# Performance work log

Hardware: AMD Instinct MI355X
Metric: run time of the kernel (lower is better)

## Reference

```python
import jax, jax.numpy as jnp
import numpy as np


def setup_inputs() -> dict:
    key = jax.random.key(0)
    kq, kk, kv = jax.random.split(key, 3)
    B, H, N, D = 2, 16, 2048, 128
    q = jax.random.normal(kq, (B, H, N, D), dtype=jnp.float32)
    k = jax.random.normal(kk, (B, H, N, D), dtype=jnp.float32)
    v = jax.random.normal(kv, (B, H, N, D), dtype=jnp.float32)
    return {"q": q, "k": k, "v": v, "num_sink": 4, "window_size": 1024}


def reference(q, k, v, num_sink, window_size):
    # Sink + sliding-window causal attention (single-device path of the SP wrapper).
    # Query i attends to key j iff j <= i AND (j < num_sink OR i - j < window_size).
    B, H, N, D = q.shape
    scale = 1.0 / np.sqrt(D).astype(np.float32)
    i = jnp.arange(N)[:, None]   # query positions
    j = jnp.arange(N)[None, :]   # key positions
    mask = (j <= i) & ((j < num_sink) | ((i - j) < window_size))  # [N, N]
    scores = jnp.einsum('bhid,bhjd->bhij', q, k) * scale          # [B,H,N,N]
    scores = jnp.where(mask, scores, jnp.finfo(scores.dtype).min)
    attn = jax.nn.softmax(scores, axis=-1)
    return jnp.einsum('bhij,bhjd->bhid', attn, v)
```

## Files before the change

### kernel.cpp

```cpp
#include <hip/hip_runtime.h>
#include <stdint.h>

#define NN 2048
#define DD 128
#define BHH 32
#define QT 64
#define KT 64

typedef short v8s __attribute__((ext_vector_type(8)));
typedef short v4s __attribute__((ext_vector_type(4)));
typedef float v4f __attribute__((ext_vector_type(4)));
typedef unsigned int u32;
typedef u32 u32x2 __attribute__((ext_vector_type(2)));
typedef u32 u32x4 __attribute__((ext_vector_type(4)));

__device__ __forceinline__ unsigned short f2bf(float x) {
  unsigned u = __builtin_bit_cast(unsigned, x);
  u += 0x7fffu + ((u >> 16) & 1u);
  return (unsigned short)(u >> 16);
}

__device__ __forceinline__ v8s cvt8(const float* __restrict__ p) {
  v8s r;
#pragma unroll
  for (int j = 0; j < 8; j++) r[j] = (short)f2bf(p[j]);
  return r;
}

__device__ __forceinline__ u32 pk2(float a, float b) {
  u32 r;
  asm("v_cvt_pk_bf16_f32 %0, %1, %2" : "=v"(r) : "v"(a), "v"(b));
  return r;
}

__global__ __launch_bounds__(256) void prep(const float* __restrict__ K, const float* __restrict__ V,
                     unsigned short* __restrict__ Kb, unsigned short* __restrict__ Vt) {
  const int z = blockIdx.z;
  const int tid = threadIdx.x;
  if (z >= BHH) {
    const int bh = z - BHH;
    const int chunk = blockIdx.y * 32 + blockIdx.x;
    size_t base = (size_t)bh * NN * DD + (size_t)chunk * 4096 + (size_t)tid * 16;
    v4f f0 = *(const v4f*)(K + base);
    v4f f1 = *(const v4f*)(K + base + 4);
    v4f f2 = *(const v4f*)(K + base + 8);
    v4f f3 = *(const v4f*)(K + base + 12);
    u32x4 w0 = { pk2(f0[0], f0[1]), pk2(f0[2], f0[3]), pk2(f1[0], f1[1]), pk2(f1[2], f1[3]) };
    u32x4 w1 = { pk2(f2[0], f2[1]), pk2(f2[2], f2[3]), pk2(f3[0], f3[1]), pk2(f3[2], f3[3]) };
    *(u32x4*)(Kb + base) = w0;
    *(u32x4*)(Kb + base + 8) = w1;
    return;
  }
  __shared__ __align__(16) unsigned short t[64 * 68];
  const int bh = z;
  const int n0 = blockIdx.x * 64, d0 = blockIdx.y * 64;
  const int c16 = tid & 15, r4 = tid >> 4;
  const float* src = V + ((size_t)bh * NN + n0 + r4 * 4) * DD + d0 + c16 * 4;
  v4f f0 = *(const v4f*)(src);
  v4f f1 = *(const v4f*)(src + DD);
  v4f f2 = *(const v4f*)(src + 2 * DD);
  v4f f3 = *(const v4f*)(src + 3 * DD);
#pragma unroll
  for (int j = 0; j < 4; j++) {
    u32x2 w = { pk2(f0[j], f1[j]), pk2(f2[j], f3[j]) };
    *(u32x2*)(t + (c16 * 4 + j) * 68 + r4 * 4) = w;
  }
  __syncthreads();
  unsigned short* dst = Vt + ((size_t)bh * DD + d0) * NN + n0;
#pragma unroll
  for (int p = 0; p < 2; p++) {
    int d = p * 32 + (tid >> 3);
    int nc = (tid & 7) * 8;
    v4s x0 = *(const v4s*)(t + d * 68 + nc);
    v4s x1 = *(const v4s*)(t + d * 68 + nc + 4);
    v8s o = { x0[0], x0[1], x0[2], x0[3], x1[0], x1[1], x1[2], x1[3] };
    *(v8s*)(dst + (size_t)d * NN + nc) = o;
  }
}

template <bool PREPPED>
__global__ __launch_bounds__(256, 3) void attn(
    const float* __restrict__ Q,
    const float* __restrict__ Kf, const unsigned short* __restrict__ Kb,
    const unsigned short* __restrict__ Vt, const float* __restrict__ Vf,
    const int* __restrict__ nsp, const int* __restrict__ wsp,
    float* __restrict__ O) {
  const int ns = nsp[0], win = wsp[0];
  const int x = blockIdx.x;
  const int xcd = x & 7, slot = x >> 3;
  const int bh = xcd + 8 * (slot / 24);
  const int jobid = slot % 24;
  int qis[2], njobs;
  if (jobid < 16) { njobs = 1; qis[0] = 31 - jobid; qis[1] = 0; }
  else { int p = jobid - 16; njobs = 2; qis[0] = 15 - p; qis[1] = p; }

  const int tid = threadIdx.x;
  const int w = tid >> 6;
  const int l = tid & 63;
  const int lo = l & 15, q4 = l >> 4;

  __shared__ __align__(16) unsigned short Kl[64 * 128];
  __shared__ __align__(16) unsigned short Vl[64 * 128];
  __shared__ __align__(16) unsigned short Pl[4 * 1024];
  unsigned short* Pw = Pl + w * 1024;
  const int prd = q4 * 128 + lo * 8;

  const float csc = 0.088388347648318447f * 1.4426950408889634f;

  const size_t koff0 = ((size_t)bh * NN + w * 16 + lo) * DD + q4 * 8;
  const unsigned short* vtb = Vt + (size_t)bh * DD * NN;

  for (int ji = 0; ji < njobs; ji++) {
    const int q0 = qis[ji] * QT;
    const int qrow0 = q0 + w * 16;
    const int qi = qrow0 + lo;

    v8s qf[4];
    {
      const float* qb = Q + ((size_t)bh * NN + qrow0 + lo) * DD + q4 * 8;
#pragma unroll
      for (int kc = 0; kc < 4; kc++) {
        v8s r;
#pragma unroll
        for (int e = 0; e < 8; e++) r[e] = (short)f2bf(qb[kc * 32 + e] * csc);
        qf[kc] = r;
      }
    }

    float lsum = 0.f;
    v4f oa[8];
#pragma unroll
    for (int nc = 0; nc < 8; nc++) oa[nc] = (v4f){0.f, 0.f, 0.f, 0.f};

    const int wstart = q0 - win + 1;
    const bool sink16 = (wstart > KT - 1) && (ns <= 16);
    const int kb_lo = sink16 ? ((wstart >> 6) << 6) : 0;
    const int kb_hi = q0 + QT;

    v8s kst[4], vst[4];
    auto stage_load = [&](int kb) {
      const size_t g = koff0 + (size_t)kb * DD;
#pragma unroll
      for (int kc = 0; kc < 4; kc++)
        kst[kc] = PREPPED ? *(const v8s*)(Kb + g + kc * 32) : cvt8(Kf + g + kc * 32);
#pragma unroll
      for (int i = 0; i < 4; i++) {
        const int f = w * 4 + i, kt = f >> 3, nc = f & 7;
        if constexpr (PREPPED) {
          vst[i] = *(const v8s*)(vtb + ((size_t)nc * 16 + lo) * NN + kb + kt * 32 + q4 * 8);
        } else {
          v8s r;
#pragma unroll
          for (int e = 0; e < 8; e++)
            r[e] = (short)f2bf(Vf[((size_t)bh * NN + kb + kt * 32 + q4 * 8 + e) * DD + nc * 16 + lo]);
          vst[i] = r;
        }
      }
    };

    stage_load(kb_lo);

    if (sink16) {
      v8s kf0[4];
      const size_t g0 = ((size_t)bh * NN + lo) * DD + q4 * 8;
#pragma unroll
      for (int kc = 0; kc < 4; kc++)
        kf0[kc] = PREPPED ? *(const v8s*)(Kb + g0 + kc * 32) : cvt8(Kf + g0 + kc * 32);
      v4f s0 = (v4f){0.f, 0.f, 0.f, 0.f};
#pragma unroll
      for (int kc = 0; kc < 4; kc++)
        s0 = __builtin_amdgcn_mfma_f32_16x16x32_bf16(kf0[kc], qf[kc], s0, 0, 0, 0);
#pragma unroll
      for (int r = 0; r < 4; r++) {
        const int kj = q4 * 4 + r;
        const bool valid = (kj < ns) && (kj <= qi);
        s0[r] = valid ? __builtin_amdgcn_exp2f(s0[r]) : 0.f;
      }
      lsum += (s0[0] + s0[1]) + (s0[2] + s0[3]);
      u32x2 pw = { pk2(s0[0], s0[1]), pk2(s0[2], s0[3]) };
      *(u32x2*)(Pw + (q4 >> 1) * 128 + lo * 8 + (q4 & 1) * 4) = pw;
      u32x2 pz = { 0u, 0u };
      *(u32x2*)(Pw + (2 + (q4 >> 1)) * 128 + lo * 8 + (q4 & 1) * 4) = pz;
      v8s pf = *(const v8s*)(Pw + prd);
#pragma unroll
      for (int nc = 0; nc < 8; nc++) {
        v8s vf;
        if constexpr (PREPPED)
          vf = *(const v8s*)(vtb + ((size_t)nc * 16 + lo) * NN + q4 * 8);
        else {
          v8s r;
#pragma unroll
          for (int e = 0; e < 8; e++)
            r[e] = (short)f2bf(Vf[((size_t)bh * NN + q4 * 8 + e) * DD + nc * 16 + lo]);
          vf = r;
        }
        oa[nc] = __builtin_amdgcn_mfma_f32_16x16x32_bf16(pf, vf, oa[nc], 0, 0, 0);
      }
    }

    for (int kb = kb_lo; kb < kb_hi; kb += KT) {
      __syncthreads();
#pragma unroll
      for (int kc = 0; kc < 4; kc++)
        *(v8s*)(Kl + (w * 4 + kc) * 512 + l * 8) = kst[kc];
#pragma unroll
      for (int i = 0; i < 4; i++)
        *(v8s*)(Vl + (w * 4 + i) * 512 + l * 8) = vst[i];
      __syncthreads();
      if (kb + KT < kb_hi) stage_load(kb + KT);

      v4f s[4];
      __builtin_amdgcn_s_setprio(1);
#pragma unroll
      for (int ct = 0; ct < 4; ct++) {
        s[ct] = (v4f){0.f, 0.f, 0.f, 0.f};
#pragma unroll
        for (int kc = 0; kc < 4; kc++) {
          v8s kf = *(const v8s*)(Kl + (ct * 4 + kc) * 512 + l * 8);
          s[ct] = __builtin_amdgcn_mfma_f32_16x16x32_bf16(kf, qf[kc], s[ct], 0, 0, 0);
        }
      }
      __builtin_amdgcn_s_setprio(0);

      const bool full = (kb + KT - 1 <= qrow0) && (kb + win >= qrow0 + 16);
      if (full) {
#pragma unroll
        for (int ct = 0; ct < 4; ct++)
#pragma unroll
          for (int r = 0; r < 4; r++) s[ct][r] = __builtin_amdgcn_exp2f(s[ct][r]);
      } else {
#pragma unroll
        for (int ct = 0; ct < 4; ct++) {
          const int kjb = kb + ct * 16 + q4 * 4;
#pragma unroll
          for (int r = 0; r < 4; r++) {
            const int kj = kjb + r;
            const bool valid = (kj <= qi) && ((kj < ns) || (qi - kj < win));
            s[ct][r] = valid ? __builtin_amdgcn_exp2f(s[ct][r]) : 0.f;
          }
        }
      }
#pragma unroll
      for (int ct = 0; ct < 4; ct++)
        lsum += (s[ct][0] + s[ct][1]) + (s[ct][2] + s[ct][3]);

#pragma unroll
      for (int ct = 0; ct < 4; ct++) {
        u32x2 pw = { pk2(s[ct][0], s[ct][1]), pk2(s[ct][2], s[ct][3]) };
        *(u32x2*)(Pw + (ct >> 1) * 512 + ((ct & 1) * 2 + (q4 >> 1)) * 128 + lo * 8 + (q4 & 1) * 4) = pw;
      }
#pragma unroll
      for (int kt = 0; kt < 2; kt++) {
        v8s pf = *(const v8s*)(Pw + kt * 512 + prd);
        __builtin_amdgcn_s_setprio(1);
#pragma unroll
        for (int nc = 0; nc < 8; nc++) {
          v8s vf = *(const v8s*)(Vl + (kt * 8 + nc) * 512 + l * 8);
          oa[nc] = __builtin_amdgcn_mfma_f32_16x16x32_bf16(pf, vf, oa[nc], 0, 0, 0);
        }
        __builtin_amdgcn_s_setprio(0);
      }
    }

    float lt = lsum;
    lt += __shfl_xor(lt, 16, 64);
    lt += __shfl_xor(lt, 32, 64);
    const float inv = 1.f / lt;
    float invr[4];
#pragma unroll
    for (int r = 0; r < 4; r++) invr[r] = __shfl(inv, (l & 48) | (q4 * 4 + r), 64);
    float* ob = O + ((size_t)bh * NN + qrow0) * DD;
#pragma unroll
    for (int nc = 0; nc < 8; nc++)
#pragma unroll
      for (int r = 0; r < 4; r++)
        ob[(size_t)(q4 * 4 + r) * DD + nc * 16 + lo] = oa[nc][r] * invr[r];
  }
}

extern "C" void kernel_launch(void* const* d_in, const int* in_sizes, int n_in,
                              void* d_out, int out_size, void* d_ws, size_t ws_size,
                              hipStream_t stream) {
  const float* q = (const float*)d_in[0];
  const float* k = (const float*)d_in[1];
  const float* v = (const float*)d_in[2];
  const int* nsp = (const int*)d_in[3];
  const int* wsp = (const int*)d_in[4];
  float* out = (float*)d_out;

  const size_t half = (size_t)BHH * NN * DD * sizeof(unsigned short);
  const int nblocks = BHH * 24;

  if (ws_size >= 2 * half) {
    unsigned short* kbf = (unsigned short*)d_ws;
    unsigned short* vt = (unsigned short*)((char*)d_ws + half);
    prep<<<dim3(32, 2, 2 * BHH), 256, 0, stream>>>(k, v, kbf, vt);
    attn<true><<<nblocks, 256, 0, stream>>>(q, k, kbf, vt, v, nsp, wsp, out);
  } else {
    attn<false><<<nblocks, 256, 0, stream>>>(q, k, nullptr, nullptr, v, nsp, wsp, out);
  }
}
```

Measured before the change: 194.0 us.

## Switch attention to 32x32x16 MFMA with two 32-row waves and register P transpose

Rewrites the attention kernel to use 32x32x16 bf16 MFMA instead of 16x16x32, with 128-thread blocks where each of two waves owns 32 query rows. The P matrix is repacked into the A-operand layout in registers via permlane32_swap instead of round-tripping through shared memory, removing the P LDS buffer. This cuts per-MFMA instruction overhead and LDS traffic but doubles per-wave register state (qf, kst/vst, accumulators) and halves threads per block, which may reduce occupancy and latency hiding.

```diff
diff --git a/kernel.cpp b/kernel.cpp
--- a/kernel.cpp
+++ b/kernel.cpp
@@ -10,6 +10,7 @@
 typedef short v8s __attribute__((ext_vector_type(8)));
 typedef short v4s __attribute__((ext_vector_type(4)));
 typedef float v4f __attribute__((ext_vector_type(4)));
+typedef float v16f __attribute__((ext_vector_type(16)));
 typedef unsigned int u32;
 typedef u32 u32x2 __attribute__((ext_vector_type(2)));
 typedef u32 u32x4 __attribute__((ext_vector_type(4)));
@@ -79,7 +80,7 @@
 }
 
 template <bool PREPPED>
-__global__ __launch_bounds__(256, 3) void attn(
+__global__ __launch_bounds__(128, 2) void attn(
     const float* __restrict__ Q,
     const float* __restrict__ Kf, const unsigned short* __restrict__ Kb,
     const unsigned short* __restrict__ Vt, const float* __restrict__ Vf,
@@ -97,62 +98,73 @@
   const int tid = threadIdx.x;
   const int w = tid >> 6;
   const int l = tid & 63;
-  const int lo = l & 15, q4 = l >> 4;
-
-  __shared__ __align__(16) unsigned short Kl[64 * 128];
-  __shared__ __align__(16) unsigned short Vl[64 * 128];
-  __shared__ __align__(16) unsigned short Pl[4 * 1024];
-  unsigned short* Pw = Pl + w * 1024;
-  const int prd = q4 * 128 + lo * 8;
+  const int m = l & 31;
+  const int hi = l >> 5;
+  const int rbase = 4 * hi;
+
+  __shared__ __align__(16) unsigned short Kl[16 * 512];
+  __shared__ __align__(16) unsigned short Vl[16 * 512];
 
   const float csc = 0.088388347648318447f * 1.4426950408889634f;
 
-  const size_t koff0 = ((size_t)bh * NN + w * 16 + lo) * DD + q4 * 8;
+  const size_t kK = ((size_t)bh * NN + w * 32 + m) * DD + hi * 8;
   const unsigned short* vtb = Vt + (size_t)bh * DD * NN;
+
+  auto mkpa = [&](float a0, float a1, float a2, float a3,
+                  float b0, float b1, float b2, float b3) -> v8s {
+    u32x2 r02 = __builtin_amdgcn_permlane32_swap(pk2(a0, a1), pk2(b0, b1), false, false);
+    u32x2 r13 = __builtin_amdgcn_permlane32_swap(pk2(a2, a3), pk2(b2, b3), false, false);
+    u32x4 pw = { r02[0], r13[0], r02[1], r13[1] };
+    return __builtin_bit_cast(v8s, pw);
+  };
 
   for (int ji = 0; ji < njobs; ji++) {
     const int q0 = qis[ji] * QT;
-    const int qrow0 = q0 + w * 16;
-    const int qi = qrow0 + lo;
-
-    v8s qf[4];
+    const int qrow0w = q0 + w * 32;
+    const int qi = qrow0w + m;
+
+    v8s qf[8];
     {
-      const float* qb = Q + ((size_t)bh * NN + qrow0 + lo) * DD + q4 * 8;
-#pragma unroll
-      for (int kc = 0; kc < 4; kc++) {
+      const float* qb = Q + ((size_t)bh * NN + qi) * DD + hi * 8;
+#pragma unroll
+      for (int kc = 0; kc < 8; kc++) {
         v8s r;
 #pragma unroll
-        for (int e = 0; e < 8; e++) r[e] = (short)f2bf(qb[kc * 32 + e] * csc);
+        for (int e = 0; e < 8; e++) r[e] = (short)f2bf(qb[kc * 16 + e] * csc);
         qf[kc] = r;
       }
     }
 
     float lsum = 0.f;
-    v4f oa[8];
-#pragma unroll
-    for (int nc = 0; nc < 8; nc++) oa[nc] = (v4f){0.f, 0.f, 0.f, 0.f};
+    v16f oa[4];
+#pragma unroll
+    for (int nc = 0; nc < 4; nc++) oa[nc] = (v16f)(0.f);
 
     const int wstart = q0 - win + 1;
     const bool sink16 = (wstart > KT - 1) && (ns <= 16);
     const int kb_lo = sink16 ? ((wstart >> 6) << 6) : 0;
     const int kb_hi = q0 + QT;
 
-    v8s kst[4], vst[4];
+    v8s kst[8], vst[8];
     auto stage_load = [&](int kb) {
-      const size_t g = koff0 + (size_t)kb * DD;
-#pragma unroll
-      for (int kc = 0; kc < 4; kc++)
-        kst[kc] = PREPPED ? *(const v8s*)(Kb + g + kc * 32) : cvt8(Kf + g + kc * 32);
-#pragma unroll
-      for (int i = 0; i < 4; i++) {
-        const int f = w * 4 + i, kt = f >> 3, nc = f & 7;
+#pragma unroll
+      for (int i = 0; i < 8; i++) {
         if constexpr (PREPPED) {
-          vst[i] = *(const v8s*)(vtb + ((size_t)nc * 16 + lo) * NN + kb + kt * 32 + q4 * 8);
+          kst[i] = *(const v8s*)(Kb + kK + (size_t)kb * DD + i * 16);
+        } else {
+          kst[i] = cvt8(Kf + kK + (size_t)kb * DD + i * 16);
+        }
+      }
+#pragma unroll
+      for (int i = 0; i < 8; i++) {
+        const int kt = w * 2 + (i >> 2), nc = i & 3;
+        if constexpr (PREPPED) {
+          vst[i] = *(const v8s*)(vtb + ((size_t)nc * 32 + m) * NN + kb + kt * 16 + hi * 8);
         } else {
           v8s r;
 #pragma unroll
           for (int e = 0; e < 8; e++)
-            r[e] = (short)f2bf(Vf[((size_t)bh * NN + kb + kt * 32 + q4 * 8 + e) * DD + nc * 16 + lo]);
+            r[e] = (short)f2bf(Vf[((size_t)bh * NN + kb + kt * 16 + hi * 8 + e) * DD + nc * 32 + m]);
           vst[i] = r;
         }
       }
@@ -161,120 +173,106 @@
     stage_load(kb_lo);
 
     if (sink16) {
-      v8s kf0[4];
-      const size_t g0 = ((size_t)bh * NN + lo) * DD + q4 * 8;
-#pragma unroll
-      for (int kc = 0; kc < 4; kc++)
-        kf0[kc] = PREPPED ? *(const v8s*)(Kb + g0 + kc * 32) : cvt8(Kf + g0 + kc * 32);
-      v4f s0 = (v4f){0.f, 0.f, 0.f, 0.f};
-#pragma unroll
-      for (int kc = 0; kc < 4; kc++)
-        s0 = __builtin_amdgcn_mfma_f32_16x16x32_bf16(kf0[kc], qf[kc], s0, 0, 0, 0);
-#pragma unroll
-      for (int r = 0; r < 4; r++) {
-        const int kj = q4 * 4 + r;
+      v8s kf0[8];
+      const size_t g0 = ((size_t)bh * NN + m) * DD + hi * 8;
+#pragma unroll
+      for (int kc = 0; kc < 8; kc++)
+        kf0[kc] = PREPPED ? *(const v8s*)(Kb + g0 + kc * 16) : cvt8(Kf + g0 + kc * 16);
+      v16f s = (v16f)(0.f);
+#pragma unroll
+      for (int kc = 0; kc < 8; kc++)
+        s = __builtin_amdgcn_mfma_f32_32x32x16_bf16(kf0[kc], qf[kc], s, 0, 0, 0);
+#pragma unroll
+      for (int reg = 0; reg < 16; reg++) {
+        const int kj = (reg & 3) + 8 * (reg >> 2) + rbase;
         const bool valid = (kj < ns) && (kj <= qi);
-        s0[r] = valid ? __builtin_amdgcn_exp2f(s0[r]) : 0.f;
-      }
-      lsum += (s0[0] + s0[1]) + (s0[2] + s0[3]);
-      u32x2 pw = { pk2(s0[0], s0[1]), pk2(s0[2], s0[3]) };
-      *(u32x2*)(Pw + (q4 >> 1) * 128 + lo * 8 + (q4 & 1) * 4) = pw;
-      u32x2 pz = { 0u, 0u };
-      *(u32x2*)(Pw + (2 + (q4 >> 1)) * 128 + lo * 8 + (q4 & 1) * 4) = pz;
-      v8s pf = *(const v8s*)(Pw + prd);
-#pragma unroll
-      for (int nc = 0; nc < 8; nc++) {
+        s[reg] = valid ? __builtin_amdgcn_exp2f(s[reg]) : 0.f;
+        lsum += s[reg];
+      }
+      v8s pa = mkpa(s[0], s[1], s[2], s[3], s[4], s[5], s[6], s[7]);
+#pragma unroll
+      for (int nc = 0; nc < 4; nc++) {
         v8s vf;
-        if constexpr (PREPPED)
-          vf = *(const v8s*)(vtb + ((size_t)nc * 16 + lo) * NN + q4 * 8);
-        else {
-          v8s r;
+        if constexpr (PREPPED) {
+          vf = *(const v8s*)(vtb + ((size_t)nc * 32 + m) * NN + hi * 8);
+        } else {
 #pragma unroll
           for (int e = 0; e < 8; e++)
-            r[e] = (short)f2bf(Vf[((size_t)bh * NN + q4 * 8 + e) * DD + nc * 16 + lo]);
-          vf = r;
-        }
-        oa[nc] = __builtin_amdgcn_mfma_f32_16x16x32_bf16(pf, vf, oa[nc], 0, 0, 0);
+            vf[e] = (short)f2bf(Vf[((size_t)bh * NN + hi * 8 + e) * DD + nc * 32 + m]);
+        }
+        oa[nc] = __builtin_amdgcn_mfma_f32_32x32x16_bf16(pa, vf, oa[nc], 0, 0, 0);
       }
     }
 
     for (int kb = kb_lo; kb < kb_hi; kb += KT) {
       __syncthreads();
 #pragma unroll
-      for (int kc = 0; kc < 4; kc++)
-        *(v8s*)(Kl + (w * 4 + kc) * 512 + l * 8) = kst[kc];
-#pragma unroll
-      for (int i = 0; i < 4; i++)
-        *(v8s*)(Vl + (w * 4 + i) * 512 + l * 8) = vst[i];
+      for (int i = 0; i < 8; i++)
+        *(v8s*)(Kl + (w * 8 + i) * 512 + l * 8) = kst[i];
+#pragma unroll
+      for (int i = 0; i < 8; i++)
+        *(v8s*)(Vl + (w * 8 + i) * 512 + l * 8) = vst[i];
       __syncthreads();
       if (kb + KT < kb_hi) stage_load(kb + KT);
 
-      v4f s[4];
-      __builtin_amdgcn_s_setprio(1);
-#pragma unroll
-      for (int ct = 0; ct < 4; ct++) {
-        s[ct] = (v4f){0.f, 0.f, 0.f, 0.f};
-#pragma unroll
-        for (int kc = 0; kc < 4; kc++) {
-          v8s kf = *(const v8s*)(Kl + (ct * 4 + kc) * 512 + l * 8);
-          s[ct] = __builtin_amdgcn_mfma_f32_16x16x32_bf16(kf, qf[kc], s[ct], 0, 0, 0);
-        }
-      }
-      __builtin_amdgcn_s_setprio(0);
-
-      const bool full = (kb + KT - 1 <= qrow0) && (kb + win >= qrow0 + 16);
-      if (full) {
-#pragma unroll
-        for (int ct = 0; ct < 4; ct++)
-#pragma unroll
-          for (int r = 0; r < 4; r++) s[ct][r] = __builtin_amdgcn_exp2f(s[ct][r]);
-      } else {
-#pragma unroll
-        for (int ct = 0; ct < 4; ct++) {
-          const int kjb = kb + ct * 16 + q4 * 4;
-#pragma unroll
-          for (int r = 0; r < 4; r++) {
-            const int kj = kjb + r;
+#pragma unroll
+      for (int ct = 0; ct < 2; ct++) {
+        v16f s = (v16f)(0.f);
+        __builtin_amdgcn_s_setprio(1);
+#pragma unroll
+        for (int kc = 0; kc < 8; kc++) {
+          v8s kfr = *(const v8s*)(Kl + (ct * 8 + kc) * 512 + l * 8);
+          s = __builtin_amdgcn_mfma_f32_32x32x16_bf16(kfr, qf[kc], s, 0, 0, 0);
+        }
+        __builtin_amdgcn_s_setprio(0);
+
+        const int kbct = kb + ct * 32;
+        const bool full = (kbct + 31 <= qrow0w) && (kbct >= qrow0w + 32 - win);
+        if (full) {
+#pragma unroll
+          for (int reg = 0; reg < 16; reg++) {
+            s[reg] = __builtin_amdgcn_exp2f(s[reg]);
+            lsum += s[reg];
+          }
+        } else {
+#pragma unroll
+          for (int reg = 0; reg < 16; reg++) {
+            const int kj = kbct + (reg & 3) + 8 * (reg >> 2) + rbase;
             const bool valid = (kj <= qi) && ((kj < ns) || (qi - kj < win));
-            s[ct][r] = valid ? __builtin_amdgcn_exp2f(s[ct][r]) : 0.f;
+            s[reg] = valid ? __builtin_amdgcn_exp2f(s[reg]) : 0.f;
+            lsum += s[reg];
           }
         }
-      }
-#pragma unroll
-      for (int ct = 0; ct < 4; ct++)
-        lsum += (s[ct][0] + s[ct][1]) + (s[ct][2] + s[ct][3]);
-
-#pragma unroll
-      for (int ct = 0; ct < 4; ct++) {
-        u32x2 pw = { pk2(s[ct][0], s[ct][1]), pk2(s[ct][2], s[ct][3]) };
-        *(u32x2*)(Pw + (ct >> 1) * 512 + ((ct & 1) * 2 + (q4 >> 1)) * 128 + lo * 8 + (q4 & 1) * 4) = pw;
-      }
-#pragma unroll
-      for (int kt = 0; kt < 2; kt++) {
-        v8s pf = *(const v8s*)(Pw + kt * 512 + prd);
+
+        v8s pa0 = mkpa(s[0], s[1], s[2], s[3], s[4], s[5], s[6], s[7]);
+        v8s pa1 = mkpa(s[8], s[9], s[10], s[11], s[12], s[13], s[14], s[15]);
+
         __builtin_amdgcn_s_setprio(1);
 #pragma unroll
-        for (int nc = 0; nc < 8; nc++) {
-          v8s vf = *(const v8s*)(Vl + (kt * 8 + nc) * 512 + l * 8);
-          oa[nc] = __builtin_amdgcn_mfma_f32_16x16x32_bf16(pf, vf, oa[nc], 0, 0, 0);
+        for (int ktl = 0; ktl < 2; ktl++) {
+          const v8s pf = ktl ? pa1 : pa0;
+          const int kt = ct * 2 + ktl;
+#pragma unroll
+          for (int nc = 0; nc < 4; nc++) {
+            v8s vfr = *(const v8s*)(Vl + (kt * 4 + nc) * 512 + l * 8);
+            oa[nc] = __builtin_amdgcn_mfma_f32_32x32x16_bf16(pf, vfr, oa[nc], 0, 0, 0);
+          }
         }
         __builtin_amdgcn_s_setprio(0);
       }
     }
 
-    float lt = lsum;
-    lt += __shfl_xor(lt, 16, 64);
-    lt += __shfl_xor(lt, 32, 64);
+    float lt = lsum + __shfl_xor(lsum, 32, 64);
     const float inv = 1.f / lt;
-    float invr[4];
-#pragma unroll
-    for (int r = 0; r < 4; r++) invr[r] = __shfl(inv, (l & 48) | (q4 * 4 + r), 64);
-    float* ob = O + ((size_t)bh * NN + qrow0) * DD;
-#pragma unroll
-    for (int nc = 0; nc < 8; nc++)
-#pragma unroll
-      for (int r = 0; r < 4; r++)
-        ob[(size_t)(q4 * 4 + r) * DD + nc * 16 + lo] = oa[nc][r] * invr[r];
+    float* ob = O + ((size_t)bh * NN + qrow0w) * DD;
+#pragma unroll
+    for (int reg = 0; reg < 16; reg++) {
+      const int row = (reg & 3) + 8 * (reg >> 2) + rbase;
+      const float iv = __shfl(inv, row, 64);
+#pragma unroll
+      for (int nc = 0; nc < 4; nc++)
+        ob[(size_t)row * DD + nc * 32 + m] = oa[nc][reg] * iv;
+    }
   }
 }
 
@@ -295,8 +293,8 @@
     unsigned short* kbf = (unsigned short*)d_ws;
     unsigned short* vt = (unsigned short*)((char*)d_ws + half);
     prep<<<dim3(32, 2, 2 * BHH), 256, 0, stream>>>(k, v, kbf, vt);
-    attn<true><<<nblocks, 256, 0, stream>>>(q, k, kbf, vt, v, nsp, wsp, out);
+    attn<true><<<nblocks, 128, 0, stream>>>(q, k, kbf, vt, v, nsp, wsp, out);
   } else {
-    attn<false><<<nblocks, 256, 0, stream>>>(q, k, nullptr, nullptr, v, nsp, wsp, out);
-  }
-}
+    attn<false><<<nblocks, 128, 0, stream>>>(q, k, nullptr, nullptr, v, nsp, wsp, out);
+  }
+}
```

Measured after the change: 196.2 us. About the same (+1.1%).
